# Optimization experiments

Measured on AMD Instinct MI355X. Metric: run time of the kernel, lower is better.

Reference implementation:

```python
import jax, jax.numpy as jnp
import numpy as np

NEG_BIG = -9e15
ALPHA = 0.2  # leakyrelu slope

N, IN_F, OUT_F = 8192, 512, 64


def setup_inputs() -> dict:
    key = jax.random.key(0)
    ks = jax.random.split(key, 7)
    return {
        "input": jax.random.normal(ks[0], (N, IN_F), dtype=jnp.float32),
        "W": jax.random.normal(ks[1], (IN_F, OUT_F), dtype=jnp.float32) * 0.05,
        "a": jax.random.normal(ks[2], (2 * OUT_F, 1), dtype=jnp.float32) * 0.1,
        "W_si": jax.random.normal(ks[3], (1, 1), dtype=jnp.float32),
        "W_ei": jax.random.normal(ks[4], (1, 1), dtype=jnp.float32),
        "adj_ad": jax.random.uniform(ks[5], (N, N), dtype=jnp.float32),
        "adj": jax.random.randint(ks[6], (N, N), 0, 2, dtype=jnp.int32),
    }


def reference(input, W, a, W_si, W_ei, adj_ad, adj):
    h = input @ W                                   # [N, F]
    F_ = h.shape[1]
    a1, a2 = a[:F_, 0], a[F_:, 0]                   # split concat projection
    # concat-score: a^T [h_i || h_j] == (h@a1)_i + (h@a2)_j, no [N,N,2F] tensor
    e = jax.nn.leaky_relu(h @ a1[:, None] + (h @ a2[:, None]).T, ALPHA)  # [N, N]
    e = jnp.abs(W_ei) * e + jnp.abs(W_si) * adj_ad
    attention = jnp.where(adj > 0, e, jnp.float32(NEG_BIG))
    attention = jax.nn.softmax(attention, axis=1)
    # dropout is identity in eval mode (training=False)
    h_prime = attention @ h                         # [N, F]
    return jax.nn.elu(h_prime)
```

## Files before the change

kernel.cpp:

```cpp
#include <hip/hip_runtime.h>
#include <math.h>

#define N 8192
#define IN_F 512
#define OUTF 64
#define TI 16
#define JT 256
#define NTILE (N / JT)
#define RS 260

typedef _Float16 f16x8 __attribute__((ext_vector_type(8)));
typedef float f32x4 __attribute__((ext_vector_type(4)));

typedef const void __attribute__((address_space(1)))* gptr_t;
typedef void __attribute__((address_space(3)))* lptr_t;

#define OFF_HT   0u
#define OFF_S    262144u
#define OFF_T    270336u
#define OFF_TMAX 278528u

__device__ __forceinline__ unsigned enc_f32(float f) {
  unsigned b = __float_as_uint(f);
  return b ^ ((unsigned)((int)b >> 31) | 0x80000000u);
}

__global__ __launch_bounds__(64) void k_precompute(
    const float* __restrict__ input, const float* __restrict__ W,
    const float* __restrict__ a, _Float16* __restrict__ hT,
    float* __restrict__ s, float* __restrict__ t) {
  const int lane = threadIdx.x;
  const int i0 = blockIdx.x * 4;

  float acc[4] = {0.f, 0.f, 0.f, 0.f};
  for (int c = 0; c < IN_F; c += 4) {
    const float w0 = W[(c + 0) * OUTF + lane];
    const float w1 = W[(c + 1) * OUTF + lane];
    const float w2 = W[(c + 2) * OUTF + lane];
    const float w3 = W[(c + 3) * OUTF + lane];
    #pragma unroll
    for (int r = 0; r < 4; r++) {
      const float4 iv = *(const float4*)(input + (size_t)(i0 + r) * IN_F + c);
      acc[r] += iv.x * w0 + iv.y * w1 + iv.z * w2 + iv.w * w3;
    }
  }

  union { _Float16 f[4]; uint2 u; } pk;
  #pragma unroll
  for (int r = 0; r < 4; r++) pk.f[r] = (_Float16)acc[r];
  *(uint2*)(hT + (size_t)lane * N + i0) = pk.u;

  const float a1v = a[lane];
  const float a2v = a[OUTF + lane];
  #pragma unroll
  for (int r = 0; r < 4; r++) {
    float sv = acc[r] * a1v;
    float tv = acc[r] * a2v;
    #pragma unroll
    for (int off = 1; off < 64; off <<= 1) {
      sv += __shfl_xor(sv, off);
      tv += __shfl_xor(tv, off);
    }
    if (lane == 0) {
      s[i0 + r] = sv;
      t[i0 + r] = tv;
    }
  }
}

__global__ __launch_bounds__(512) void k_tmax(const float* __restrict__ t,
                                              unsigned* __restrict__ tmax) {
  __shared__ float red[8];
  const int tid = threadIdx.x;
  float m = t[blockIdx.x * 512 + tid];
  #pragma unroll
  for (int off = 1; off < 64; off <<= 1) m = fmaxf(m, __shfl_xor(m, off));
  if ((tid & 63) == 0) red[tid >> 6] = m;
  __syncthreads();
  if (tid == 0) {
    #pragma unroll
    for (int w = 1; w < 8; w++) m = fmaxf(m, red[w]);
    atomicMax(tmax, enc_f32(m));
  }
}

__global__ __launch_bounds__(384, 3) void k_attn(
    const _Float16* __restrict__ hT, const float* __restrict__ s,
    const float* __restrict__ t, const unsigned* __restrict__ tmaxp,
    const float* __restrict__ W_si, const float* __restrict__ W_ei,
    const float* __restrict__ adj_ad, const int* __restrict__ adj,
    float* __restrict__ out) {
  __shared__ __align__(16) float bufA[2][TI * RS];
  __shared__ __align__(16) int   bufM[2][TI * RS];

  const int tid = threadIdx.x;
  const int wave = tid >> 6;
  const int lane = tid & 63;
  const int q = lane >> 4;
  const int m = lane & 15;
  const int i0 = blockIdx.x * TI;

  const float aei = fabsf(W_ei[0]);
  const float asi = fabsf(W_si[0]);
  const unsigned te = *tmaxp;
  const float tm = __uint_as_float((te & 0x80000000u) ? (te ^ 0x80000000u) : ~te);

  const float sr = s[i0 + m];
  const float xm = sr + tm;
  const float Mr = aei * fmaxf(xm, 0.2f * xm) + asi;

  float S = 0.f;
  f32x4 acc[4];
  #pragma unroll
  for (int nb = 0; nb < 4; nb++) acc[nb] = (f32x4){0.f, 0.f, 0.f, 0.f};

  const int p = wave - 4;

  #define STAGE(b, j0s)                                                        \
    {                                                                          \
      _Pragma("unroll") for (int g = 0; g < 8; g++) {                          \
        const int row = p * 8 + g;                                             \
        __builtin_amdgcn_global_load_lds(                                      \
            (gptr_t)(adj_ad + (size_t)(i0 + row) * N + (j0s) + lane * 4),      \
            (lptr_t)&bufA[b][row * RS], 16, 0, 0);                             \
      }                                                                        \
      _Pragma("unroll") for (int g = 0; g < 8; g++) {                          \
        const int row = p * 8 + g;                                             \
        __builtin_amdgcn_global_load_lds(                                      \
            (gptr_t)(adj + (size_t)(i0 + row) * N + (j0s) + lane * 4),         \
            (lptr_t)&bufM[b][row * RS], 16, 0, 0);                             \
      }                                                                        \
    }

  if (wave >= 4) STAGE(0, 0);

  #pragma unroll 1
  for (int k = 0; k < NTILE; k++) {
    __syncthreads();

    if (wave >= 4) {
      if (k + 1 < NTILE) STAGE((k + 1) & 1, (k + 1) * JT);
    } else {
      const int buf = k & 1;
      const int j0 = k * JT;
      #pragma unroll
      for (int ck = 0; ck < 2; ck++) {
        const int kc = 2 * wave + ck;
        const int cb = j0 + kc * 32 + q * 8;
        const int lb = m * RS + kc * 32 + q * 8;

        const float4 tfa = *(const float4*)&t[cb];
        const float4 tfb = *(const float4*)&t[cb + 4];
        const float4 a0 = *(const float4*)&bufA[buf][lb];
        const float4 a1 = *(const float4*)&bufA[buf][lb + 4];
        const int4 k0 = *(const int4*)&bufM[buf][lb];
        const int4 k1 = *(const int4*)&bufM[buf][lb + 4];

        const float ad[8] = {a0.x, a0.y, a0.z, a0.w, a1.x, a1.y, a1.z, a1.w};
        const int mk[8] = {k0.x, k0.y, k0.z, k0.w, k1.x, k1.y, k1.z, k1.w};
        const float tv[8] = {tfa.x, tfa.y, tfa.z, tfa.w,
                             tfb.x, tfb.y, tfb.z, tfb.w};

        f16x8 fa;
        #pragma unroll
        for (int e = 0; e < 8; e++) {
          const float x = sr + tv[e];
          const float ee = aei * fmaxf(x, 0.2f * x) + asi * ad[e];
          const float pv = (mk[e] > 0) ? __expf(ee - Mr) : 0.f;
          S += pv;
          fa[e] = (_Float16)pv;
        }
        #pragma unroll
        for (int nb = 0; nb < 4; nb++) {
          const f16x8 fb = *(const f16x8*)&hT[(size_t)(nb * 16 + m) * N + cb];
          acc[nb] = __builtin_amdgcn_mfma_f32_16x16x32_f16(fa, fb, acc[nb],
                                                           0, 0, 0);
        }
      }
    }
  }

  float* aLDS = &bufA[0][0];
  float* sLDS = (float*)&bufM[0][0];

  if (wave < 4) {
    sLDS[wave * 64 + lane] = S;
    #pragma unroll
    for (int nb = 0; nb < 4; nb++) {
      #pragma unroll
      for (int reg = 0; reg < 4; reg++) {
        aLDS[wave * 1024 + (q * 4 + reg) * 64 + nb * 16 + m] = acc[nb][reg];
      }
    }
  }
  __syncthreads();

  if (wave < 4) {
    #pragma unroll
    for (int ii = 0; ii < 4; ii++) {
      const int e = tid + 256 * ii;
      const int r = e >> 6;
      const int f = e & 63;
      float num = 0.f, den = 0.f;
      #pragma unroll
      for (int w = 0; w < 4; w++) {
        num += aLDS[w * 1024 + r * 64 + f];
        #pragma unroll
        for (int qq = 0; qq < 4; qq++) den += sLDS[w * 64 + qq * 16 + r];
      }
      const float x = num / den;
      out[(size_t)(i0 + r) * OUTF + f] = x > 0.f ? x : expm1f(x);
    }
  }
}

extern "C" void kernel_launch(void* const* d_in, const int* in_sizes, int n_in,
                              void* d_out, int out_size, void* d_ws, size_t ws_size,
                              hipStream_t stream) {
  const float* input  = (const float*)d_in[0];
  const float* W      = (const float*)d_in[1];
  const float* a      = (const float*)d_in[2];
  const float* W_si   = (const float*)d_in[3];
  const float* W_ei   = (const float*)d_in[4];
  const float* adj_ad = (const float*)d_in[5];
  const int*   adj    = (const int*)d_in[6];
  float* out = (float*)d_out;
  float* ws  = (float*)d_ws;

  _Float16* hT   = (_Float16*)(ws + OFF_HT);
  float* s       = ws + OFF_S;
  float* t       = ws + OFF_T;
  unsigned* tmax = (unsigned*)(ws + OFF_TMAX);

  hipMemsetAsync(tmax, 0, 4, stream);
  k_precompute<<<N / 4, 64, 0, stream>>>(input, W, a, hT, s, t);
  k_tmax<<<N / 512, 512, 0, stream>>>(t, tmax);
  k_attn<<<N / TI, 384, 0, stream>>>(hT, s, t, tmax, W_si, W_ei,
                                     adj_ad, adj, out);
}
```

Before: 582.9 us.

## Replace LDS producer-wave staging with direct register-prefetched global loads

The attention kernel drops its two producer waves and the double-buffered LDS staging of adj_ad/adj via global_load_lds. Each of the four compute waves now loads adj_ad, adj and t straight into registers, with software prefetch one chunk ahead. Column chunks are rotated per block so blocks start at different offsets. This removes the per-tile __syncthreads and the LDS traffic, and LDS use drops so more blocks fit per CU. In exchange it relies on register prefetch alone to hide HBM latency, and each lane's loads cover only 32 contiguous bytes per row, which may coalesce less well than the previous staged loads.

```diff
diff --git a/kernel.cpp b/kernel.cpp
--- a/kernel.cpp
+++ b/kernel.cpp
@@ -5,15 +5,9 @@
 #define IN_F 512
 #define OUTF 64
 #define TI 16
-#define JT 256
-#define NTILE (N / JT)
-#define RS 260
 
 typedef _Float16 f16x8 __attribute__((ext_vector_type(8)));
 typedef float f32x4 __attribute__((ext_vector_type(4)));
-
-typedef const void __attribute__((address_space(1)))* gptr_t;
-typedef void __attribute__((address_space(3)))* lptr_t;
 
 #define OFF_HT   0u
 #define OFF_S    262144u
@@ -84,14 +78,14 @@
   }
 }
 
-__global__ __launch_bounds__(384, 3) void k_attn(
+__global__ __launch_bounds__(256, 4) void k_attn(
     const _Float16* __restrict__ hT, const float* __restrict__ s,
     const float* __restrict__ t, const unsigned* __restrict__ tmaxp,
     const float* __restrict__ W_si, const float* __restrict__ W_ei,
     const float* __restrict__ adj_ad, const int* __restrict__ adj,
     float* __restrict__ out) {
-  __shared__ __align__(16) float bufA[2][TI * RS];
-  __shared__ __align__(16) int   bufM[2][TI * RS];
+  __shared__ float aLDS[4 * 1024];
+  __shared__ float sLDS[4 * 64];
 
   const int tid = threadIdx.x;
   const int wave = tid >> 6;
@@ -99,6 +93,7 @@
   const int q = lane >> 4;
   const int m = lane & 15;
   const int i0 = blockIdx.x * TI;
+  const int off = blockIdx.x & 15;
 
   const float aei = fabsf(W_ei[0]);
   const float asi = fabsf(W_si[0]);
@@ -114,103 +109,93 @@
   #pragma unroll
   for (int nb = 0; nb < 4; nb++) acc[nb] = (f32x4){0.f, 0.f, 0.f, 0.f};
 
-  const int p = wave - 4;
-
-  #define STAGE(b, j0s)                                                        \
-    {                                                                          \
-      _Pragma("unroll") for (int g = 0; g < 8; g++) {                          \
-        const int row = p * 8 + g;                                             \
-        __builtin_amdgcn_global_load_lds(                                      \
-            (gptr_t)(adj_ad + (size_t)(i0 + row) * N + (j0s) + lane * 4),      \
-            (lptr_t)&bufA[b][row * RS], 16, 0, 0);                             \
-      }                                                                        \
-      _Pragma("unroll") for (int g = 0; g < 8; g++) {                          \
-        const int row = p * 8 + g;                                             \
-        __builtin_amdgcn_global_load_lds(                                      \
-            (gptr_t)(adj + (size_t)(i0 + row) * N + (j0s) + lane * 4),         \
-            (lptr_t)&bufM[b][row * RS], 16, 0, 0);                             \
-      }                                                                        \
-    }
-
-  if (wave >= 4) STAGE(0, 0);
-
+  const size_t rowA = (size_t)(i0 + m) * N;
+
+  auto CB = [&](int c) -> int {
+    return ((((((c >> 2) + off) & 15) << 4) + (wave << 2) + (c & 3)) << 5) +
+           (q << 3);
+  };
+
+  struct Pf { float4 a0, a1, t0, t1; int4 k0, k1; };
+
+  auto LOADC = [&](int c) -> Pf {
+    const int cb = CB(c);
+    Pf p;
+    p.a0 = *(const float4*)(adj_ad + rowA + cb);
+    p.a1 = *(const float4*)(adj_ad + rowA + cb + 4);
+    p.k0 = *(const int4*)(adj + rowA + cb);
+    p.k1 = *(const int4*)(adj + rowA + cb + 4);
+    p.t0 = *(const float4*)(t + cb);
+    p.t1 = *(const float4*)(t + cb + 4);
+    return p;
+  };
+
+  auto LHT = [&](int c, f16x8* fb) {
+    const int cb = CB(c);
+    #pragma unroll
+    for (int nb = 0; nb < 4; nb++)
+      fb[nb] = *(const f16x8*)(hT + (size_t)(nb * 16 + m) * N + cb);
+  };
+
+  auto COMPUTE = [&](const Pf& p, const f16x8* fb) {
+    const float ad[8] = {p.a0.x, p.a0.y, p.a0.z, p.a0.w,
+                         p.a1.x, p.a1.y, p.a1.z, p.a1.w};
+    const int mk[8] = {p.k0.x, p.k0.y, p.k0.z, p.k0.w,
+                       p.k1.x, p.k1.y, p.k1.z, p.k1.w};
+    const float tv[8] = {p.t0.x, p.t0.y, p.t0.z, p.t0.w,
+                         p.t1.x, p.t1.y, p.t1.z, p.t1.w};
+    f16x8 fa;
+    #pragma unroll
+    for (int e = 0; e < 8; e++) {
+      const float x = sr + tv[e];
+      const float ee = aei * fmaxf(x, 0.2f * x) + asi * ad[e];
+      const float pv = (mk[e] > 0) ? __expf(ee - Mr) : 0.f;
+      S += pv;
+      fa[e] = (_Float16)pv;
+    }
+    #pragma unroll
+    for (int nb = 0; nb < 4; nb++)
+      acc[nb] = __builtin_amdgcn_mfma_f32_16x16x32_f16(fa, fb[nb], acc[nb],
+                                                       0, 0, 0);
+  };
+
+  Pf pa = LOADC(0);
   #pragma unroll 1
-  for (int k = 0; k < NTILE; k++) {
-    __syncthreads();
-
-    if (wave >= 4) {
-      if (k + 1 < NTILE) STAGE((k + 1) & 1, (k + 1) * JT);
-    } else {
-      const int buf = k & 1;
-      const int j0 = k * JT;
+  for (int c = 0; c < 64; c += 2) {
+    f16x8 fbA[4];
+    LHT(c, fbA);
+    Pf pb = LOADC(c + 1);
+    COMPUTE(pa, fbA);
+    f16x8 fbB[4];
+    LHT(c + 1, fbB);
+    pa = LOADC((c + 2) & 63);
+    COMPUTE(pb, fbB);
+  }
+
+  sLDS[wave * 64 + lane] = S;
+  #pragma unroll
+  for (int nb = 0; nb < 4; nb++) {
+    #pragma unroll
+    for (int reg = 0; reg < 4; reg++) {
+      aLDS[wave * 1024 + (q * 4 + reg) * 64 + nb * 16 + m] = acc[nb][reg];
+    }
+  }
+  __syncthreads();
+
+  #pragma unroll
+  for (int ii = 0; ii < 4; ii++) {
+    const int e = tid + 256 * ii;
+    const int r = e >> 6;
+    const int f = e & 63;
+    float num = 0.f, den = 0.f;
+    #pragma unroll
+    for (int w = 0; w < 4; w++) {
+      num += aLDS[w * 1024 + r * 64 + f];
       #pragma unroll
-      for (int ck = 0; ck < 2; ck++) {
-        const int kc = 2 * wave + ck;
-        const int cb = j0 + kc * 32 + q * 8;
-        const int lb = m * RS + kc * 32 + q * 8;
-
-        const float4 tfa = *(const float4*)&t[cb];
-        const float4 tfb = *(const float4*)&t[cb + 4];
-        const float4 a0 = *(const float4*)&bufA[buf][lb];
-        const float4 a1 = *(const float4*)&bufA[buf][lb + 4];
-        const int4 k0 = *(const int4*)&bufM[buf][lb];
-        const int4 k1 = *(const int4*)&bufM[buf][lb + 4];
-
-        const float ad[8] = {a0.x, a0.y, a0.z, a0.w, a1.x, a1.y, a1.z, a1.w};
-        const int mk[8] = {k0.x, k0.y, k0.z, k0.w, k1.x, k1.y, k1.z, k1.w};
-        const float tv[8] = {tfa.x, tfa.y, tfa.z, tfa.w,
-                             tfb.x, tfb.y, tfb.z, tfb.w};
-
-        f16x8 fa;
-        #pragma unroll
-        for (int e = 0; e < 8; e++) {
-          const float x = sr + tv[e];
-          const float ee = aei * fmaxf(x, 0.2f * x) + asi * ad[e];
-          const float pv = (mk[e] > 0) ? __expf(ee - Mr) : 0.f;
-          S += pv;
-          fa[e] = (_Float16)pv;
-        }
-        #pragma unroll
-        for (int nb = 0; nb < 4; nb++) {
-          const f16x8 fb = *(const f16x8*)&hT[(size_t)(nb * 16 + m) * N + cb];
-          acc[nb] = __builtin_amdgcn_mfma_f32_16x16x32_f16(fa, fb, acc[nb],
-                                                           0, 0, 0);
-        }
-      }
-    }
-  }
-
-  float* aLDS = &bufA[0][0];
-  float* sLDS = (float*)&bufM[0][0];
-
-  if (wave < 4) {
-    sLDS[wave * 64 + lane] = S;
-    #pragma unroll
-    for (int nb = 0; nb < 4; nb++) {
-      #pragma unroll
-      for (int reg = 0; reg < 4; reg++) {
-        aLDS[wave * 1024 + (q * 4 + reg) * 64 + nb * 16 + m] = acc[nb][reg];
-      }
-    }
-  }
-  __syncthreads();
-
-  if (wave < 4) {
-    #pragma unroll
-    for (int ii = 0; ii < 4; ii++) {
-      const int e = tid + 256 * ii;
-      const int r = e >> 6;
-      const int f = e & 63;
-      float num = 0.f, den = 0.f;
-      #pragma unroll
-      for (int w = 0; w < 4; w++) {
-        num += aLDS[w * 1024 + r * 64 + f];
-        #pragma unroll
-        for (int qq = 0; qq < 4; qq++) den += sLDS[w * 64 + qq * 16 + r];
-      }
-      const float x = num / den;
-      out[(size_t)(i0 + r) * OUTF + f] = x > 0.f ? x : expm1f(x);
-    }
+      for (int qq = 0; qq < 4; qq++) den += sLDS[w * 64 + qq * 16 + r];
+    }
+    const float x = num / den;
+    out[(size_t)(i0 + r) * OUTF + f] = x > 0.f ? x : expm1f(x);
   }
 }
 
@@ -235,6 +220,6 @@
   hipMemsetAsync(tmax, 0, 4, stream);
   k_precompute<<<N / 4, 64, 0, stream>>>(input, W, a, hT, s, t);
   k_tmax<<<N / 512, 512, 0, stream>>>(t, tmax);
-  k_attn<<<N / TI, 384, 0, stream>>>(hT, s, t, tmax, W_si, W_ei,
+  k_attn<<<N / TI, 256, 0, stream>>>(hT, s, t, tmax, W_si, W_ei,
                                      adj_ad, adj, out);
 }
```

After: 705.7 us. +21.1%, slower.

## Replace producer/consumer waves with unified 8-wave, 4-buffer software pipeline

Applied to the files above, without the earlier changes.

Removes the dedicated loader waves so all 8 waves both issue async global-to-LDS loads and compute, each handling 2 rows of staging and one 32-column chunk. Uses a 4-deep LDS ring with explicit vmcnt waits and raw barriers, and register double-buffers the hT/t loads one tile ahead. Intended to increase memory-level parallelism and compute throughput per block. The larger LDS footprint limits occupancy to one block per CU, and the hand-counted vmcnt values are fragile at the tail.

```diff
diff --git a/kernel.cpp b/kernel.cpp
--- a/kernel.cpp
+++ b/kernel.cpp
@@ -8,6 +8,7 @@
 #define JT 256
 #define NTILE (N / JT)
 #define RS 260
+#define NBUF 4
 
 typedef _Float16 f16x8 __attribute__((ext_vector_type(8)));
 typedef float f32x4 __attribute__((ext_vector_type(4)));
@@ -84,17 +85,17 @@
   }
 }
 
-__global__ __launch_bounds__(384, 3) void k_attn(
+__global__ __launch_bounds__(512) void k_attn(
     const _Float16* __restrict__ hT, const float* __restrict__ s,
     const float* __restrict__ t, const unsigned* __restrict__ tmaxp,
     const float* __restrict__ W_si, const float* __restrict__ W_ei,
     const float* __restrict__ adj_ad, const int* __restrict__ adj,
     float* __restrict__ out) {
-  __shared__ __align__(16) float bufA[2][TI * RS];
-  __shared__ __align__(16) int   bufM[2][TI * RS];
+  __shared__ __align__(16) float bufA[NBUF][TI * RS];
+  __shared__ __align__(16) int   bufM[NBUF][TI * RS];
 
   const int tid = threadIdx.x;
-  const int wave = tid >> 6;
+  const int w = tid >> 6;
   const int lane = tid & 63;
   const int q = lane >> 4;
   const int m = lane & 15;
@@ -114,103 +115,116 @@
   #pragma unroll
   for (int nb = 0; nb < 4; nb++) acc[nb] = (f32x4){0.f, 0.f, 0.f, 0.f};
 
-  const int p = wave - 4;
-
-  #define STAGE(b, j0s)                                                        \
-    {                                                                          \
-      _Pragma("unroll") for (int g = 0; g < 8; g++) {                          \
-        const int row = p * 8 + g;                                             \
-        __builtin_amdgcn_global_load_lds(                                      \
-            (gptr_t)(adj_ad + (size_t)(i0 + row) * N + (j0s) + lane * 4),      \
-            (lptr_t)&bufA[b][row * RS], 16, 0, 0);                             \
-      }                                                                        \
-      _Pragma("unroll") for (int g = 0; g < 8; g++) {                          \
-        const int row = p * 8 + g;                                             \
-        __builtin_amdgcn_global_load_lds(                                      \
-            (gptr_t)(adj + (size_t)(i0 + row) * N + (j0s) + lane * 4),         \
-            (lptr_t)&bufM[b][row * RS], 16, 0, 0);                             \
-      }                                                                        \
-    }
-
-  if (wave >= 4) STAGE(0, 0);
+  const int r0 = w * 2;
+  const size_t gR0 = (size_t)(i0 + r0) * N;
+  const int cbl = w * 32 + q * 8;
+  const int lb = m * RS + cbl;
+
+  #define STAGE(kt)                                                           \
+    {                                                                         \
+      const int b_ = (kt) & (NBUF - 1);                                       \
+      const int j0_ = (kt) * JT;                                              \
+      __builtin_amdgcn_global_load_lds(                                       \
+          (gptr_t)(adj_ad + gR0 + j0_ + lane * 4),                            \
+          (lptr_t)&bufA[b_][r0 * RS], 16, 0, 0);                              \
+      __builtin_amdgcn_global_load_lds(                                       \
+          (gptr_t)(adj_ad + gR0 + N + j0_ + lane * 4),                        \
+          (lptr_t)&bufA[b_][(r0 + 1) * RS], 16, 0, 0);                        \
+      __builtin_amdgcn_global_load_lds(                                       \
+          (gptr_t)(adj + gR0 + j0_ + lane * 4),                               \
+          (lptr_t)&bufM[b_][r0 * RS], 16, 0, 0);                              \
+      __builtin_amdgcn_global_load_lds(                                       \
+          (gptr_t)(adj + gR0 + N + j0_ + lane * 4),                           \
+          (lptr_t)&bufM[b_][(r0 + 1) * RS], 16, 0, 0);                        \
+    }
+
+  #define RLOAD(kt, H, T0, T1)                                                \
+    {                                                                         \
+      const int cb_ = (kt) * JT + cbl;                                        \
+      _Pragma("unroll") for (int nb = 0; nb < 4; nb++)                        \
+          H[nb] = *(const f16x8*)(hT + (size_t)(nb * 16 + m) * N + cb_);      \
+      T0 = *(const float4*)(t + cb_);                                         \
+      T1 = *(const float4*)(t + cb_ + 4);                                     \
+    }
+
+  #define COMPUTE(kt, H, T0, T1)                                              \
+    {                                                                         \
+      const int b_ = (kt) & (NBUF - 1);                                       \
+      const float4 a0 = *(const float4*)&bufA[b_][lb];                        \
+      const float4 a1 = *(const float4*)&bufA[b_][lb + 4];                    \
+      const int4 k0 = *(const int4*)&bufM[b_][lb];                            \
+      const int4 k1 = *(const int4*)&bufM[b_][lb + 4];                        \
+      const float ad[8] = {a0.x, a0.y, a0.z, a0.w, a1.x, a1.y, a1.z, a1.w};   \
+      const int mk[8] = {k0.x, k0.y, k0.z, k0.w, k1.x, k1.y, k1.z, k1.w};     \
+      const float tv[8] = {T0.x, T0.y, T0.z, T0.w, T1.x, T1.y, T1.z, T1.w};   \
+      f16x8 fa;                                                               \
+      _Pragma("unroll") for (int e = 0; e < 8; e++) {                         \
+        const float x = sr + tv[e];                                           \
+        const float ee = aei * fmaxf(x, 0.2f * x) + asi * ad[e];              \
+        const float pv = (mk[e] > 0) ? __expf(ee - Mr) : 0.f;                 \
+        S += pv;                                                              \
+        fa[e] = (_Float16)pv;                                                 \
+      }                                                                       \
+      _Pragma("unroll") for (int nb = 0; nb < 4; nb++)                        \
+          acc[nb] = __builtin_amdgcn_mfma_f32_16x16x32_f16(fa, H[nb],         \
+                                                           acc[nb], 0, 0, 0);\
+    }
+
+  #define PHASE_SYNC(n)                                                       \
+    asm volatile("s_waitcnt vmcnt(" #n ")" ::: "memory");                     \
+    __builtin_amdgcn_sched_barrier(0);                                        \
+    __builtin_amdgcn_s_barrier();                                             \
+    __builtin_amdgcn_sched_barrier(0);
+
+  f16x8 hA[4], hB[4];
+  float4 tA0, tA1, tB0, tB1;
+
+  STAGE(0);
+  RLOAD(0, hA, tA0, tA1);
+  STAGE(1);
+  STAGE(2);
+  PHASE_SYNC(8);
 
   #pragma unroll 1
-  for (int k = 0; k < NTILE; k++) {
-    __syncthreads();
-
-    if (wave >= 4) {
-      if (k + 1 < NTILE) STAGE((k + 1) & 1, (k + 1) * JT);
-    } else {
-      const int buf = k & 1;
-      const int j0 = k * JT;
-      #pragma unroll
-      for (int ck = 0; ck < 2; ck++) {
-        const int kc = 2 * wave + ck;
-        const int cb = j0 + kc * 32 + q * 8;
-        const int lb = m * RS + kc * 32 + q * 8;
-
-        const float4 tfa = *(const float4*)&t[cb];
-        const float4 tfb = *(const float4*)&t[cb + 4];
-        const float4 a0 = *(const float4*)&bufA[buf][lb];
-        const float4 a1 = *(const float4*)&bufA[buf][lb + 4];
-        const int4 k0 = *(const int4*)&bufM[buf][lb];
-        const int4 k1 = *(const int4*)&bufM[buf][lb + 4];
-
-        const float ad[8] = {a0.x, a0.y, a0.z, a0.w, a1.x, a1.y, a1.z, a1.w};
-        const int mk[8] = {k0.x, k0.y, k0.z, k0.w, k1.x, k1.y, k1.z, k1.w};
-        const float tv[8] = {tfa.x, tfa.y, tfa.z, tfa.w,
-                             tfb.x, tfb.y, tfb.z, tfb.w};
-
-        f16x8 fa;
-        #pragma unroll
-        for (int e = 0; e < 8; e++) {
-          const float x = sr + tv[e];
-          const float ee = aei * fmaxf(x, 0.2f * x) + asi * ad[e];
-          const float pv = (mk[e] > 0) ? __expf(ee - Mr) : 0.f;
-          S += pv;
-          fa[e] = (_Float16)pv;
-        }
-        #pragma unroll
-        for (int nb = 0; nb < 4; nb++) {
-          const f16x8 fb = *(const f16x8*)&hT[(size_t)(nb * 16 + m) * N + cb];
-          acc[nb] = __builtin_amdgcn_mfma_f32_16x16x32_f16(fa, fb, acc[nb],
-                                                           0, 0, 0);
-        }
-      }
-    }
+  for (int k = 0; k < NTILE; k += 2) {
+    RLOAD(k + 1, hB, tB0, tB1);
+    if (k + 3 < NTILE) STAGE(k + 3);
+    COMPUTE(k, hA, tA0, tA1);
+    PHASE_SYNC(14);
+
+    if (k + 2 < NTILE) RLOAD(k + 2, hA, tA0, tA1);
+    if (k + 4 < NTILE) STAGE(k + 4);
+    COMPUTE(k + 1, hB, tB0, tB1);
+    PHASE_SYNC(14);
   }
 
   float* aLDS = &bufA[0][0];
   float* sLDS = (float*)&bufM[0][0];
 
-  if (wave < 4) {
-    sLDS[wave * 64 + lane] = S;
-    #pragma unroll
-    for (int nb = 0; nb < 4; nb++) {
+  sLDS[w * 64 + lane] = S;
+  #pragma unroll
+  for (int nb = 0; nb < 4; nb++) {
+    #pragma unroll
+    for (int reg = 0; reg < 4; reg++) {
+      aLDS[w * 1024 + (q * 4 + reg) * 64 + nb * 16 + m] = acc[nb][reg];
+    }
+  }
+  __syncthreads();
+
+  #pragma unroll
+  for (int ii = 0; ii < 2; ii++) {
+    const int e = tid + 512 * ii;
+    const int r = e >> 6;
+    const int f = e & 63;
+    float num = 0.f, den = 0.f;
+    #pragma unroll
+    for (int ww = 0; ww < 8; ww++) {
+      num += aLDS[ww * 1024 + r * 64 + f];
       #pragma unroll
-      for (int reg = 0; reg < 4; reg++) {
-        aLDS[wave * 1024 + (q * 4 + reg) * 64 + nb * 16 + m] = acc[nb][reg];
-      }
-    }
-  }
-  __syncthreads();
-
-  if (wave < 4) {
-    #pragma unroll
-    for (int ii = 0; ii < 4; ii++) {
-      const int e = tid + 256 * ii;
-      const int r = e >> 6;
-      const int f = e & 63;
-      float num = 0.f, den = 0.f;
-      #pragma unroll
-      for (int w = 0; w < 4; w++) {
-        num += aLDS[w * 1024 + r * 64 + f];
-        #pragma unroll
-        for (int qq = 0; qq < 4; qq++) den += sLDS[w * 64 + qq * 16 + r];
-      }
-      const float x = num / den;
-      out[(size_t)(i0 + r) * OUTF + f] = x > 0.f ? x : expm1f(x);
-    }
+      for (int qq = 0; qq < 4; qq++) den += sLDS[ww * 64 + qq * 16 + r];
+    }
+    const float x = num / den;
+    out[(size_t)(i0 + r) * OUTF + f] = x > 0.f ? x : expm1f(x);
   }
 }
 
@@ -235,6 +249,6 @@
   hipMemsetAsync(tmax, 0, 4, stream);
   k_precompute<<<N / 4, 64, 0, stream>>>(input, W, a, hT, s, t);
   k_tmax<<<N / 512, 512, 0, stream>>>(t, tmax);
-  k_attn<<<N / TI, 384, 0, stream>>>(hT, s, t, tmax, W_si, W_ei,
+  k_attn<<<N / TI, 512, 0, stream>>>(hT, s, t, tmax, W_si, W_ei,
                                      adj_ad, adj, out);
 }
```

New measurement: 571.6 us. Within noise of the previous version (-1.9%).
